# Performance work log

Hardware: AMD Instinct MI355X
Metric: run time of the kernel (lower is better)

Reference implementation:

```python
import jax, jax.numpy as jnp
import numpy as np

B, L, P, C = 8, 4, 1024, 256
NH, NS = 8, 4
HD = C // NH  # 32
LEVEL_HW = [(64, 64), (32, 32), (16, 16), (8, 8)]


def setup_inputs() -> dict:
    key = jax.random.key(0)
    ks = jax.random.split(key, 14)
    inp = {
        "x": jax.random.normal(ks[0], (B, L, P, C), jnp.float32),
        # reference points are grid_sample coords in [-1, 1]
        "ref": jax.random.uniform(ks[1], (B, L, P, 2), jnp.float32, -0.9, 0.9),
    }
    for i, (h, w) in enumerate(LEVEL_HW):
        inp[f"feat{i}"] = jax.random.normal(ks[2 + i], (B, C, h, w), jnp.float32)
    inp["w_attn"] = jax.random.normal(ks[6], (C, NH * NS), jnp.float32) * 0.02
    inp["b_attn"] = jax.random.normal(ks[7], (NH * NS,), jnp.float32) * 0.02
    inp["w_off"] = jax.random.normal(ks[8], (C, 2 * NH * NS), jnp.float32) * 0.02
    inp["b_off"] = jax.random.normal(ks[9], (2 * NH * NS,), jnp.float32) * 0.02
    inp["embed_w"] = jax.random.normal(ks[10], (L, C, HD), jnp.float32) * 0.02
    inp["embed_b"] = jax.random.normal(ks[11], (L, HD), jnp.float32) * 0.02
    return inp


def grid_sample_bilinear(feat, grid):
    """torch.F.grid_sample(mode='bilinear', padding_mode='zeros', align_corners=True).
    feat: (B, C, H, W); grid: (B, Gh, Gw, 2) with (x, y) in [-1, 1].
    Returns (B, Gh, Gw, C)  (already permuted vs torch's (B, C, Gh, Gw))."""
    Bn, Cn, H, W = feat.shape
    fx = (grid[..., 0] + 1.0) * 0.5 * (W - 1)  # align_corners=True mapping
    fy = (grid[..., 1] + 1.0) * 0.5 * (H - 1)
    x0f = jnp.floor(fx)
    y0f = jnp.floor(fy)
    x0 = x0f.astype(jnp.int32)
    y0 = y0f.astype(jnp.int32)
    x1 = x0 + 1
    y1 = y0 + 1
    wx1 = fx - x0f
    wy1 = fy - y0f
    wx0 = 1.0 - wx1
    wy0 = 1.0 - wy1
    feat_hwc = jnp.transpose(feat, (0, 2, 3, 1))  # (B, H, W, C)

    def gather(yi, xi):
        valid = ((yi >= 0) & (yi < H) & (xi >= 0) & (xi < W)).astype(feat.dtype)
        yc = jnp.clip(yi, 0, H - 1)
        xc = jnp.clip(xi, 0, W - 1)
        v = jax.vmap(lambda f, y, x: f[y, x])(feat_hwc, yc, xc)  # (B, Gh, Gw, C)
        return v * valid[..., None]

    out = (gather(y0, x0) * (wy0 * wx0)[..., None]
           + gather(y0, x1) * (wy0 * wx1)[..., None]
           + gather(y1, x0) * (wy1 * wx0)[..., None]
           + gather(y1, x1) * (wy1 * wx1)[..., None])
    return out


def reference(x, ref, feat0, feat1, feat2, feat3,
              w_attn, b_attn, w_off, b_off, embed_w, embed_b):
    feats = [feat0, feat1, feat2, feat3]
    b, l, p, c = x.shape
    # attention weights: softmax over samples
    weights = jax.nn.softmax((x @ w_attn + b_attn).reshape(b, l, p, NH, NS), axis=-1)
    # sampling offsets, squashed by tanh
    offsets = jnp.tanh((x @ w_off + b_off).reshape(b, l, p, NH * NS, 2))
    pos = offsets + ref[:, :, :, None, :]  # (b, l, p, NH*NS, 2)
    sampled = []
    for i, f in enumerate(feats):
        s = grid_sample_bilinear(f, pos[:, i])  # (b, p, NH*NS, C_l)
        sampled.append(s @ embed_w[i] + embed_b[i])  # (b, p, NH*NS, HD)
    fs = jnp.stack(sampled, axis=1).reshape(b, l, p, NH, NS, HD)
    out = (weights[..., None] * fs).sum(axis=-2).reshape(b, l, p, NH * HD)
    return out
```

## Files before the change

kernel.cpp:

```cpp
#include <hip/hip_runtime.h>
#include <math.h>

#define B_   8
#define L_   4
#define P_   1024
#define C_   256
#define NH_  8
#define NS_  4
#define HD_  32

typedef _Float16 half8 __attribute__((ext_vector_type(8)));
typedef _Float16 half4 __attribute__((ext_vector_type(4)));
typedef float    f32x4 __attribute__((ext_vector_type(4)));

#define G_F     0u
#define SAMP_F  1392640u
#define WU_F    5586944u
#define ET_F    5611520u

__constant__ const int kGoff[4] = {0, 1048576, 1310720, 1376256};

#define XH2 72
#define LGS 100
#define FTS 40
#define ETS 264
#define NG_GPROJ 680

__global__ void k0_conv(const float* __restrict__ wa, const float* __restrict__ wo,
                        const float* __restrict__ embed_w,
                        _Float16* __restrict__ WuT, _Float16* __restrict__ ET16) {
  const int bx = blockIdx.x, t = threadIdx.x;
  if (bx < 96) {
    const int n = bx;
    const float v = (n < 32) ? wa[t * 32 + n] : wo[t * 64 + (n - 32)];
    WuT[n * 256 + t] = (_Float16)v;
  } else {
    const int i0 = (bx - 96) * 1024 + t * 4;
    const int l = i0 >> 13, rem = i0 & 8191;
    const int c = rem >> 5, e0 = rem & 31;
    const float4 v = *(const float4*)(embed_w + i0);
    _Float16* d = ET16 + l * 8192 + c;
    d[(e0 + 0) * 256] = (_Float16)v.x;
    d[(e0 + 1) * 256] = (_Float16)v.y;
    d[(e0 + 2) * 256] = (_Float16)v.z;
    d[(e0 + 3) * 256] = (_Float16)v.w;
  }
}

__global__ __launch_bounds__(256) void stage1(
    const float* __restrict__ f0, const float* __restrict__ f1,
    const float* __restrict__ f2, const float* __restrict__ f3,
    const _Float16* __restrict__ ET16, _Float16* __restrict__ g16,
    const float* __restrict__ x,
    const float* __restrict__ ref,
    const _Float16* __restrict__ WuT,
    const float* __restrict__ ba, const float* __restrict__ bo,
    float4* __restrict__ samp4)
{
  __shared__ float4 smraw4[1600];
  const int t = threadIdx.x;
  const int bx = blockIdx.x;
  const int lane = t & 63, wv = t >> 6;
  const int lr = lane & 15, kg = lane >> 4;

  if (bx < NG_GPROJ) {
    _Float16* eT  = (_Float16*)smraw4;
    _Float16* flT = eT + 32 * ETS;
    const int b = bx / 85;
    int sub = bx - b * 85, l, tile;
    const float* src;
    if (sub < 64)      { l = 0; tile = sub;      src = f0; }
    else if (sub < 80) { l = 1; tile = sub - 64; src = f1; }
    else if (sub < 84) { l = 2; tile = sub - 80; src = f2; }
    else               { l = 3; tile = 0;        src = f3; }
    const int Wl = 64 >> l, S = Wl * Wl;
    const int s0 = tile * 64;

    {
      const float4* es = (const float4*)(ET16 + (size_t)l * 8192);
      #pragma unroll
      for (int q8 = 0; q8 < 4; ++q8) {
        const int q = q8 * 256 + t;
        const int e = q >> 5, c8 = q & 31;
        *(float4*)(eT + e * ETS + c8 * 8) = es[q];
      }
    }

    const float* sb = src + (size_t)b * C_ * S + s0;
    const int sl = t & 63, cb = (t >> 6) * 8;

    f32x4 acc[2];
    acc[0] = (f32x4){0.f, 0.f, 0.f, 0.f};
    acc[1] = (f32x4){0.f, 0.f, 0.f, 0.f};

    for (int chunk = 0; chunk < 8; ++chunk) {
      const int c0 = chunk * 32;
      if (chunk) __syncthreads();
      {
        float v[8];
        #pragma unroll
        for (int i = 0; i < 8; ++i) v[i] = sb[(size_t)(c0 + cb + i) * S + sl];
        const half8 hv = {(_Float16)v[0], (_Float16)v[1], (_Float16)v[2], (_Float16)v[3],
                          (_Float16)v[4], (_Float16)v[5], (_Float16)v[6], (_Float16)v[7]};
        *(half8*)(flT + sl * FTS + cb) = hv;
      }
      __syncthreads();
      const half8 a  = *(const half8*)(flT + (wv * 16 + lr) * FTS + kg * 8);
      const half8 b0 = *(const half8*)(eT + lr * ETS + c0 + kg * 8);
      const half8 b1 = *(const half8*)(eT + (16 + lr) * ETS + c0 + kg * 8);
      acc[0] = __builtin_amdgcn_mfma_f32_16x16x32_f16(a, b0, acc[0], 0, 0, 0);
      acc[1] = __builtin_amdgcn_mfma_f32_16x16x32_f16(a, b1, acc[1], 0, 0, 0);
    }

    _Float16* gb = g16 + kGoff[l] + ((size_t)b * S + s0 + wv * 16 + kg * 4) * 32;
    #pragma unroll
    for (int nt = 0; nt < 2; ++nt)
      #pragma unroll
      for (int r = 0; r < 4; ++r)
        gb[r * 32 + nt * 16 + lr] = (_Float16)acc[nt][r];
    return;
  }

  _Float16* smx = (_Float16*)smraw4;
  _Float16* smw = (_Float16*)smraw4 + 64 * XH2;
  float*    lg  = (float*)smraw4;

  const int blk = bx - NG_GPROJ;
  const int gp0 = blk * 64;

  f32x4 acc[6];
  #pragma unroll
  for (int nt = 0; nt < 6; ++nt) acc[nt] = (f32x4){0.f, 0.f, 0.f, 0.f};

  #pragma unroll
  for (int chunk = 0; chunk < 4; ++chunk) {
    const int c0 = chunk * 64;
    if (chunk) __syncthreads();
    {
      const int pt = t >> 2, q = t & 3;
      const float4* src = (const float4*)(x + (size_t)(gp0 + pt) * 256 + c0 + q * 16);
      const float4 v0 = src[0], v1 = src[1], v2 = src[2], v3 = src[3];
      _Float16* dst = smx + pt * XH2 + q * 16;
      *(half8*)dst = (half8){(_Float16)v0.x, (_Float16)v0.y, (_Float16)v0.z, (_Float16)v0.w,
                             (_Float16)v1.x, (_Float16)v1.y, (_Float16)v1.z, (_Float16)v1.w};
      *(half8*)(dst + 8) = (half8){(_Float16)v2.x, (_Float16)v2.y, (_Float16)v2.z, (_Float16)v2.w,
                                   (_Float16)v3.x, (_Float16)v3.y, (_Float16)v3.z, (_Float16)v3.w};
    }
    {
      #pragma unroll
      for (int q = 0; q < 3; ++q) {
        const int idx = q * 256 + t;
        const int n = idx >> 3, col8 = idx & 7;
        *(float4*)(smw + n * XH2 + col8 * 8) =
            *(const float4*)(WuT + (size_t)n * 256 + c0 + col8 * 8);
      }
    }
    __syncthreads();

    #pragma unroll
    for (int ks = 0; ks < 2; ++ks) {
      const half8 a = *(const half8*)(smx + (wv * 16 + lr) * XH2 + ks * 32 + kg * 8);
      #pragma unroll
      for (int nt = 0; nt < 6; ++nt) {
        const half8 bf = *(const half8*)(smw + (nt * 16 + lr) * XH2 + ks * 32 + kg * 8);
        acc[nt] = __builtin_amdgcn_mfma_f32_16x16x32_f16(a, bf, acc[nt], 0, 0, 0);
      }
    }
  }
  __syncthreads();

  #pragma unroll
  for (int nt = 0; nt < 6; ++nt) {
    const int n = nt * 16 + lr;
    const float bv = (n < 32) ? ba[n] : bo[n - 32];
    #pragma unroll
    for (int r = 0; r < 4; ++r)
      lg[(wv * 16 + kg * 4 + r) * LGS + n] = acc[nt][r] + bv;
  }
  __syncthreads();

  #pragma unroll
  for (int k = 0; k < 8; ++k) {
    const int slot = k * 256 + t;
    const int pp = slot >> 5, j = slot & 31;
    const int gp = gp0 + pp;
    const int l = (gp >> 10) & 3;
    const int Wl = 64 >> l;
    const float* lgp = lg + pp * LGS;
    const int h4 = (j >> 2) * 4;
    const float l0 = lgp[h4], l1 = lgp[h4 + 1], l2 = lgp[h4 + 2], l3 = lgp[h4 + 3];
    const float m = fmaxf(fmaxf(l0, l1), fmaxf(l2, l3));
    const float e0 = expf(l0 - m), e1 = expf(l1 - m), e2 = expf(l2 - m), e3 = expf(l3 - m);
    const float inv = 1.f / (e0 + e1 + e2 + e3);
    const float es[4] = {e0, e1, e2, e3};
    const float wj = es[j & 3] * inv;
    const float ox = tanhf(lgp[32 + 2 * j])     + ref[(size_t)gp * 2];
    const float oy = tanhf(lgp[32 + 2 * j + 1]) + ref[(size_t)gp * 2 + 1];
    const float sc = 0.5f * (float)(Wl - 1);
    samp4[(size_t)gp * 32 + j] = make_float4(wj, (ox + 1.f) * sc, (oy + 1.f) * sc, 0.f);
  }
}

__global__ __launch_bounds__(256) void k3_main(
    const _Float16* __restrict__ g16,
    const float4* __restrict__ samp4,
    const float* __restrict__ embed_b,
    float* __restrict__ out)
{
  __shared__ int4   tofs[256];
  __shared__ float4 tws[256];
  const int t = threadIdx.x, blk = blockIdx.x;
  const int gp0 = blk * 8;
  const int l = (gp0 >> 10) & 3, b = gp0 >> 12;
  const int Wl = 64 >> l;
  const int gbase = kGoff[l] + b * Wl * Wl * 32;

  {
    const float4 s = samp4[(size_t)gp0 * 32 + t];
    const float fx = s.y, fy = s.z;
    const float x0f = floorf(fx), y0f = floorf(fy);
    const int x0 = (int)x0f, y0 = (int)y0f, x1 = x0 + 1, y1 = y0 + 1;
    const float wx1 = fx - x0f, wy1 = fy - y0f;
    const float wx0 = 1.f - wx1, wy0 = 1.f - wy1;
    const float xv0 = (x0 >= 0 && x0 < Wl) ? 1.f : 0.f;
    const float xv1 = (x1 >= 0 && x1 < Wl) ? 1.f : 0.f;
    const float yv0 = (y0 >= 0 && y0 < Wl) ? 1.f : 0.f;
    const float yv1 = (y1 >= 0 && y1 < Wl) ? 1.f : 0.f;
    const int x0c = min(max(x0, 0), Wl - 1), x1c = min(max(x1, 0), Wl - 1);
    const int y0c = min(max(y0, 0), Wl - 1), y1c = min(max(y1, 0), Wl - 1);
    tofs[t] = make_int4(gbase + (y0c * Wl + x0c) * 32,
                        gbase + (y0c * Wl + x1c) * 32,
                        gbase + (y1c * Wl + x0c) * 32,
                        gbase + (y1c * Wl + x1c) * 32);
    const float w = s.x;
    tws[t] = make_float4(w * wy0 * wx0 * yv0 * xv0,
                         w * wy0 * wx1 * yv0 * xv1,
                         w * wy1 * wx0 * yv1 * xv0,
                         w * wy1 * wx1 * yv1 * xv1);
  }
  __syncthreads();

  const int dq = t & 3, h = (t >> 2) & 7, pt = t >> 5;
  float a[8];
  {
    const float4* bb = (const float4*)(embed_b + l * 32 + dq * 8);
    const float4 b0 = bb[0], b1 = bb[1];
    a[0] = b0.x; a[1] = b0.y; a[2] = b0.z; a[3] = b0.w;
    a[4] = b1.x; a[5] = b1.y; a[6] = b1.z; a[7] = b1.w;
  }
  #pragma unroll
  for (int s = 0; s < 4; ++s) {
    const int slot = pt * 32 + h * 4 + s;
    const int4   o = tofs[slot];
    const float4 w = tws[slot];
    const half8 v00 = *(const half8*)(g16 + o.x + dq * 8);
    const half8 v01 = *(const half8*)(g16 + o.y + dq * 8);
    const half8 v10 = *(const half8*)(g16 + o.z + dq * 8);
    const half8 v11 = *(const half8*)(g16 + o.w + dq * 8);
    #pragma unroll
    for (int j = 0; j < 8; ++j)
      a[j] += w.x * (float)v00[j] + w.y * (float)v01[j]
            + w.z * (float)v10[j] + w.w * (float)v11[j];
  }
  float* od = out + (size_t)(gp0 + pt) * 256 + h * 32 + dq * 8;
  ((float4*)od)[0] = make_float4(a[0], a[1], a[2], a[3]);
  ((float4*)od)[1] = make_float4(a[4], a[5], a[6], a[7]);
}

extern "C" void kernel_launch(void* const* d_in, const int* in_sizes, int n_in,
                              void* d_out, int out_size, void* d_ws, size_t ws_size,
                              hipStream_t stream) {
  const float* x      = (const float*)d_in[0];
  const float* ref    = (const float*)d_in[1];
  const float* w_attn = (const float*)d_in[6];
  const float* b_attn = (const float*)d_in[7];
  const float* w_off  = (const float*)d_in[8];
  const float* b_off  = (const float*)d_in[9];
  const float* emb_w  = (const float*)d_in[10];
  const float* emb_b  = (const float*)d_in[11];
  float* ws  = (float*)d_ws;
  float* out = (float*)d_out;

  _Float16* g16   = (_Float16*)(ws + G_F);
  float4*   samp4 = (float4*)(ws + SAMP_F);
  _Float16* WuT   = (_Float16*)(ws + WU_F);
  _Float16* ET16  = (_Float16*)(ws + ET_F);

  k0_conv<<<128, 256, 0, stream>>>(w_attn, w_off, emb_w, WuT, ET16);

  stage1<<<NG_GPROJ + B_ * L_ * P_ / 64, 256, 0, stream>>>(
      (const float*)d_in[2], (const float*)d_in[3],
      (const float*)d_in[4], (const float*)d_in[5], ET16, g16,
      x, ref, WuT, b_attn, b_off, samp4);

  k3_main<<<B_ * L_ * P_ / 8, 256, 0, stream>>>(g16, samp4, emb_b, out);
}
```

Before: 52.12 us.

## Prefetch all feature loads into registers and load projection operands directly from global

In the feature-projection blocks, all 64 feature values per thread are now loaded into registers up front, before the embedding tile is staged. The fp16 staging buffer is double-buffered so that only one barrier per chunk is needed and global latency is overlapped. In the x-projection blocks, x rows are read straight into MFMA A fragments and the weight fragments are read directly from global/L2, which drops the LDS staging and its barriers. The cost is much higher register pressure (64 floats plus 16 float4) and more scattered global loads for the weights.

Result: slower. 59.50 us (+14.1%).

```diff
diff --git a/kernel.cpp b/kernel.cpp
--- a/kernel.cpp
+++ b/kernel.cpp
@@ -20,7 +20,6 @@
 
 __constant__ const int kGoff[4] = {0, 1048576, 1310720, 1376256};
 
-#define XH2 72
 #define LGS 100
 #define FTS 40
 #define ETS 264
@@ -57,7 +56,7 @@
     const float* __restrict__ ba, const float* __restrict__ bo,
     float4* __restrict__ samp4)
 {
-  __shared__ float4 smraw4[1600];
+  __shared__ float4 smraw4[1696];
   const int t = threadIdx.x;
   const int bx = blockIdx.x;
   const int lane = t & 63, wv = t >> 6;
@@ -76,6 +75,16 @@
     const int Wl = 64 >> l, S = Wl * Wl;
     const int s0 = tile * 64;
 
+    const float* sb = src + (size_t)b * C_ * S + s0;
+    const int sl = t & 63, cb = (t >> 6) * 8;
+
+    float v[64];
+    #pragma unroll
+    for (int g = 0; g < 8; ++g)
+      #pragma unroll
+      for (int i = 0; i < 8; ++i)
+        v[g * 8 + i] = sb[(size_t)(g * 32 + cb + i) * S + sl];
+
     {
       const float4* es = (const float4*)(ET16 + (size_t)l * 8192);
       #pragma unroll
@@ -85,27 +94,21 @@
         *(float4*)(eT + e * ETS + c8 * 8) = es[q];
       }
     }
-
-    const float* sb = src + (size_t)b * C_ * S + s0;
-    const int sl = t & 63, cb = (t >> 6) * 8;
+    __syncthreads();
 
     f32x4 acc[2];
     acc[0] = (f32x4){0.f, 0.f, 0.f, 0.f};
     acc[1] = (f32x4){0.f, 0.f, 0.f, 0.f};
 
-    for (int chunk = 0; chunk < 8; ++chunk) {
-      const int c0 = chunk * 32;
-      if (chunk) __syncthreads();
-      {
-        float v[8];
-        #pragma unroll
-        for (int i = 0; i < 8; ++i) v[i] = sb[(size_t)(c0 + cb + i) * S + sl];
-        const half8 hv = {(_Float16)v[0], (_Float16)v[1], (_Float16)v[2], (_Float16)v[3],
-                          (_Float16)v[4], (_Float16)v[5], (_Float16)v[6], (_Float16)v[7]};
-        *(half8*)(flT + sl * FTS + cb) = hv;
-      }
+    #pragma unroll
+    for (int c = 0; c < 8; ++c) {
+      const int c0 = c * 32;
+      _Float16* fb = flT + (c & 1) * (64 * FTS);
+      const half8 hv = {(_Float16)v[c*8+0], (_Float16)v[c*8+1], (_Float16)v[c*8+2], (_Float16)v[c*8+3],
+                        (_Float16)v[c*8+4], (_Float16)v[c*8+5], (_Float16)v[c*8+6], (_Float16)v[c*8+7]};
+      *(half8*)(fb + sl * FTS + cb) = hv;
       __syncthreads();
-      const half8 a  = *(const half8*)(flT + (wv * 16 + lr) * FTS + kg * 8);
+      const half8 a  = *(const half8*)(fb + (wv * 16 + lr) * FTS + kg * 8);
       const half8 b0 = *(const half8*)(eT + lr * ETS + c0 + kg * 8);
       const half8 b1 = *(const half8*)(eT + (16 + lr) * ETS + c0 + kg * 8);
       acc[0] = __builtin_amdgcn_mfma_f32_16x16x32_f16(a, b0, acc[0], 0, 0, 0);
@@ -121,53 +124,40 @@
     return;
   }
 
-  _Float16* smx = (_Float16*)smraw4;
-  _Float16* smw = (_Float16*)smraw4 + 64 * XH2;
-  float*    lg  = (float*)smraw4;
-
+  float* lg = (float*)smraw4;
   const int blk = bx - NG_GPROJ;
   const int gp0 = blk * 64;
 
+  const float* xrow = x + (size_t)(gp0 + wv * 16 + lr) * 256;
+  float4 xa[16];
+  #pragma unroll
+  for (int f = 0; f < 8; ++f) {
+    const int koff = (f >> 1) * 64 + (f & 1) * 32 + kg * 8;
+    const float4* p = (const float4*)(xrow + koff);
+    xa[2 * f]     = p[0];
+    xa[2 * f + 1] = p[1];
+  }
+  half8 af[8];
+  #pragma unroll
+  for (int f = 0; f < 8; ++f) {
+    const float4 u = xa[2 * f], w2 = xa[2 * f + 1];
+    af[f] = (half8){(_Float16)u.x,  (_Float16)u.y,  (_Float16)u.z,  (_Float16)u.w,
+                    (_Float16)w2.x, (_Float16)w2.y, (_Float16)w2.z, (_Float16)w2.w};
+  }
+
   f32x4 acc[6];
   #pragma unroll
   for (int nt = 0; nt < 6; ++nt) acc[nt] = (f32x4){0.f, 0.f, 0.f, 0.f};
 
   #pragma unroll
-  for (int chunk = 0; chunk < 4; ++chunk) {
-    const int c0 = chunk * 64;
-    if (chunk) __syncthreads();
-    {
-      const int pt = t >> 2, q = t & 3;
-      const float4* src = (const float4*)(x + (size_t)(gp0 + pt) * 256 + c0 + q * 16);
-      const float4 v0 = src[0], v1 = src[1], v2 = src[2], v3 = src[3];
-      _Float16* dst = smx + pt * XH2 + q * 16;
-      *(half8*)dst = (half8){(_Float16)v0.x, (_Float16)v0.y, (_Float16)v0.z, (_Float16)v0.w,
-                             (_Float16)v1.x, (_Float16)v1.y, (_Float16)v1.z, (_Float16)v1.w};
-      *(half8*)(dst + 8) = (half8){(_Float16)v2.x, (_Float16)v2.y, (_Float16)v2.z, (_Float16)v2.w,
-                                   (_Float16)v3.x, (_Float16)v3.y, (_Float16)v3.z, (_Float16)v3.w};
+  for (int f = 0; f < 8; ++f) {
+    const int koff = (f >> 1) * 64 + (f & 1) * 32 + kg * 8;
+    #pragma unroll
+    for (int nt = 0; nt < 6; ++nt) {
+      const half8 bf = *(const half8*)(WuT + (size_t)(nt * 16 + lr) * 256 + koff);
+      acc[nt] = __builtin_amdgcn_mfma_f32_16x16x32_f16(af[f], bf, acc[nt], 0, 0, 0);
     }
-    {
-      #pragma unroll
-      for (int q = 0; q < 3; ++q) {
-        const int idx = q * 256 + t;
-        const int n = idx >> 3, col8 = idx & 7;
-        *(float4*)(smw + n * XH2 + col8 * 8) =
-            *(const float4*)(WuT + (size_t)n * 256 + c0 + col8 * 8);
-      }
-    }
-    __syncthreads();
-
-    #pragma unroll
-    for (int ks = 0; ks < 2; ++ks) {
-      const half8 a = *(const half8*)(smx + (wv * 16 + lr) * XH2 + ks * 32 + kg * 8);
-      #pragma unroll
-      for (int nt = 0; nt < 6; ++nt) {
-        const half8 bf = *(const half8*)(smw + (nt * 16 + lr) * XH2 + ks * 32 + kg * 8);
-        acc[nt] = __builtin_amdgcn_mfma_f32_16x16x32_f16(a, bf, acc[nt], 0, 0, 0);
-      }
-    }
-  }
-  __syncthreads();
+  }
 
   #pragma unroll
   for (int nt = 0; nt < 6; ++nt) {
```

## Double-buffer feature tile, prefetch next chunk in registers, read embed weights from global

Applied to the files above, without the earlier changes.

The per-level feature projection blocks stop staging the embed weight matrix in shared memory and instead load the B fragments straight from global (L2-resident) memory. The feature chunk loop is fully unrolled with register prefetch of the next chunk and a two-slot shared buffer, which removes one barrier per iteration. This is meant to overlap global loads with MFMA work and cut LDS setup and sync cost. The trade-off is more global traffic for the weight fragments and higher register pressure.

Result: faster. 50.88 us (-2.4%).

```diff
diff --git a/kernel.cpp b/kernel.cpp
--- a/kernel.cpp
+++ b/kernel.cpp
@@ -23,7 +23,6 @@
 #define XH2 72
 #define LGS 100
 #define FTS 40
-#define ETS 264
 #define NG_GPROJ 680
 
 __global__ void k0_conv(const float* __restrict__ wa, const float* __restrict__ wo,
@@ -64,8 +63,7 @@
   const int lr = lane & 15, kg = lane >> 4;
 
   if (bx < NG_GPROJ) {
-    _Float16* eT  = (_Float16*)smraw4;
-    _Float16* flT = eT + 32 * ETS;
+    _Float16* flT = (_Float16*)smraw4;
     const int b = bx / 85;
     int sub = bx - b * 85, l, tile;
     const float* src;
@@ -76,48 +74,45 @@
     const int Wl = 64 >> l, S = Wl * Wl;
     const int s0 = tile * 64;
 
-    {
-      const float4* es = (const float4*)(ET16 + (size_t)l * 8192);
+    const float* sb = src + (size_t)b * C_ * S + s0;
+    const _Float16* ETl = ET16 + (size_t)l * 8192;
+    const int sl = t & 63, cb = (t >> 6) * 8;
+
+    float vcur[8], vnext[8];
+    #pragma unroll
+    for (int i = 0; i < 8; ++i) vnext[i] = sb[(size_t)(cb + i) * S + sl];
+
+    f32x4 acc0 = (f32x4){0.f, 0.f, 0.f, 0.f};
+    f32x4 acc1 = (f32x4){0.f, 0.f, 0.f, 0.f};
+
+    #pragma unroll
+    for (int c = 0; c < 8; ++c) {
+      const int c0 = c * 32;
       #pragma unroll
-      for (int q8 = 0; q8 < 4; ++q8) {
-        const int q = q8 * 256 + t;
-        const int e = q >> 5, c8 = q & 31;
-        *(float4*)(eT + e * ETS + c8 * 8) = es[q];
+      for (int i = 0; i < 8; ++i) vcur[i] = vnext[i];
+      if (c < 7) {
+        #pragma unroll
+        for (int i = 0; i < 8; ++i)
+          vnext[i] = sb[(size_t)(c0 + 32 + cb + i) * S + sl];
       }
-    }
-
-    const float* sb = src + (size_t)b * C_ * S + s0;
-    const int sl = t & 63, cb = (t >> 6) * 8;
-
-    f32x4 acc[2];
-    acc[0] = (f32x4){0.f, 0.f, 0.f, 0.f};
-    acc[1] = (f32x4){0.f, 0.f, 0.f, 0.f};
-
-    for (int chunk = 0; chunk < 8; ++chunk) {
-      const int c0 = chunk * 32;
-      if (chunk) __syncthreads();
-      {
-        float v[8];
-        #pragma unroll
-        for (int i = 0; i < 8; ++i) v[i] = sb[(size_t)(c0 + cb + i) * S + sl];
-        const half8 hv = {(_Float16)v[0], (_Float16)v[1], (_Float16)v[2], (_Float16)v[3],
-                          (_Float16)v[4], (_Float16)v[5], (_Float16)v[6], (_Float16)v[7]};
-        *(half8*)(flT + sl * FTS + cb) = hv;
-      }
+      _Float16* fb = flT + (c & 1) * (64 * FTS);
+      const half8 hv = {(_Float16)vcur[0], (_Float16)vcur[1], (_Float16)vcur[2], (_Float16)vcur[3],
+                        (_Float16)vcur[4], (_Float16)vcur[5], (_Float16)vcur[6], (_Float16)vcur[7]};
+      *(half8*)(fb + sl * FTS + cb) = hv;
       __syncthreads();
-      const half8 a  = *(const half8*)(flT + (wv * 16 + lr) * FTS + kg * 8);
-      const half8 b0 = *(const half8*)(eT + lr * ETS + c0 + kg * 8);
-      const half8 b1 = *(const half8*)(eT + (16 + lr) * ETS + c0 + kg * 8);
-      acc[0] = __builtin_amdgcn_mfma_f32_16x16x32_f16(a, b0, acc[0], 0, 0, 0);
-      acc[1] = __builtin_amdgcn_mfma_f32_16x16x32_f16(a, b1, acc[1], 0, 0, 0);
+      const half8 a  = *(const half8*)(fb + (wv * 16 + lr) * FTS + kg * 8);
+      const half8 b0 = *(const half8*)(ETl + (size_t)lr * 256 + c0 + kg * 8);
+      const half8 b1 = *(const half8*)(ETl + (size_t)(16 + lr) * 256 + c0 + kg * 8);
+      acc0 = __builtin_amdgcn_mfma_f32_16x16x32_f16(a, b0, acc0, 0, 0, 0);
+      acc1 = __builtin_amdgcn_mfma_f32_16x16x32_f16(a, b1, acc1, 0, 0, 0);
     }
 
     _Float16* gb = g16 + kGoff[l] + ((size_t)b * S + s0 + wv * 16 + kg * 4) * 32;
     #pragma unroll
-    for (int nt = 0; nt < 2; ++nt)
-      #pragma unroll
-      for (int r = 0; r < 4; ++r)
-        gb[r * 32 + nt * 16 + lr] = (_Float16)acc[nt][r];
+    for (int r = 0; r < 4; ++r) {
+      gb[r * 32 + lr]      = (_Float16)acc0[r];
+      gb[r * 32 + 16 + lr] = (_Float16)acc1[r];
+    }
     return;
   }
 
```
